# Optimization experiments

Hardware: AMD Instinct MI355X
Metric: run time of the kernel (lower is better)

## Reference

```python
import jax, jax.numpy as jnp
import numpy as np

DIM = 1024
HIDDEN = 4096
NUM_EXPERTS = 8
TOP_K = 2


def setup_inputs() -> dict:
    key = jax.random.key(0)
    ks = jax.random.split(key, 7)
    x = jax.random.normal(ks[0], (4, 2048, DIM), dtype=jnp.float32)
    # router Linear(dim, num_experts)
    Wr = jax.random.normal(ks[1], (DIM, NUM_EXPERTS), dtype=jnp.float32) / np.sqrt(DIM)
    br = jnp.zeros((NUM_EXPERTS,), dtype=jnp.float32)
    # stacked expert weights: Linear(dim, hidden) -> GELU -> Linear(hidden, dim)
    W1 = jax.random.normal(ks[2], (NUM_EXPERTS, DIM, HIDDEN), dtype=jnp.float32) / np.sqrt(DIM)
    b1 = jnp.zeros((NUM_EXPERTS, HIDDEN), dtype=jnp.float32)
    W2 = jax.random.normal(ks[3], (NUM_EXPERTS, HIDDEN, DIM), dtype=jnp.float32) / np.sqrt(HIDDEN)
    b2 = jnp.zeros((NUM_EXPERTS, DIM), dtype=jnp.float32)
    return {"x": x, "Wr": Wr, "br": br, "W1": W1, "b1": b1, "W2": W2, "b2": b2}


def reference(x, Wr, br, W1, b1, W2, b2):
    # router: g_x = W_e x ; p = softmax(g_x)
    logits = jnp.einsum('bsd,de->bse', x, Wr) + br            # [B,S,E]
    probs = jax.nn.softmax(logits, axis=-1)
    topk_probs, topk_idx = jax.lax.top_k(probs, TOP_K)        # [B,S,K]
    # dense compute-all-experts (faithful to torch.stack over experts)
    h = jnp.einsum('bsd,edh->bseh', x, W1) + b1               # [B,S,E,H]
    h = jax.nn.gelu(h, approximate=False)                      # torch nn.GELU default = exact erf
    expert_out = jnp.einsum('bseh,ehd->bsed', h, W2) + b2     # [B,S,E,D]
    # gather top-k expert outputs and mix
    selected = jnp.take_along_axis(expert_out, topk_idx[..., None], axis=2)  # [B,S,K,D]
    mixed = jnp.sum(topk_probs[..., None] * selected, axis=2)                # [B,S,D]
    return mixed, logits, probs, topk_idx, topk_probs
```

## Files before the change

### kernel.cpp

```cpp
#include <hip/hip_runtime.h>
#include <hip/hip_bf16.h>
#include <math.h>
#include <stdint.h>

#define DIMD 1024
#define HIDDEN 4096
#define NE 8
#define TOPK_ 2
#define T_TOKENS 8192
#define NROWS (T_TOKENS * TOPK_)
#define BM 128
#define BN 256
#define BK 64
#define MAXTILES (NROWS / BM + NE)
#define TGS 8
#define SPLITK 2

typedef __bf16 bf16_t;
typedef __bf16 bf16x8 __attribute__((ext_vector_type(8)));
typedef float f32x4 __attribute__((ext_vector_type(4)));

__device__ __forceinline__ void glds16(const void* g, void* l) {
    __builtin_amdgcn_global_load_lds(
        (const __attribute__((address_space(1))) unsigned int*)g,
        (__attribute__((address_space(3))) unsigned int*)l, 16, 0, 0);
}

__device__ __forceinline__ bf16x8 ldfrag(const char* lds_, int row, int kelem) {
    int byte = row * 128 + ((kelem * 2) ^ ((row & 7) << 4));
    return *reinterpret_cast<const bf16x8*>(lds_ + byte);
}

__device__ __forceinline__ int xcd_contig(int bid, int nwg) {
    int xcd = bid & 7;
    int lid = bid >> 3;
    int q = nwg >> 3, r = nwg & 7;
    int base = (xcd < r) ? xcd * (q + 1) : r * (q + 1) + (xcd - r) * q;
    return base + lid;
}

#define STAGE6(kb) do { \
    glds16(pa0 + (kb), lds + wid * 1024); \
    glds16(pa1 + (kb), lds + 8192 + wid * 1024); \
    glds16(pb0 + (kb), lds + 16384 + wid * 1024); \
    glds16(pb1 + (kb), lds + 16384 + 8192 + wid * 1024); \
    glds16(pb2 + (kb), lds + 16384 + 16384 + wid * 1024); \
    glds16(pb3 + (kb), lds + 16384 + 24576 + wid * 1024); \
} while (0)

#define COMPUTE() do { \
    _Pragma("unroll") for (int ks_ = 0; ks_ < 2; ++ks_) { \
        int kk_ = ks_ * 32 + k4; \
        bf16x8 b_[4], a_[4]; \
        _Pragma("unroll") for (int n_ = 0; n_ < 4; ++n_) \
            b_[n_] = ldfrag(lds + 16384, wc + n_ * 16 + rr, kk_); \
        _Pragma("unroll") for (int m_ = 0; m_ < 4; ++m_) \
            a_[m_] = ldfrag(lds, wr + m_ * 16 + rr, kk_); \
        _Pragma("unroll") for (int m_ = 0; m_ < 4; ++m_) \
        _Pragma("unroll") for (int n_ = 0; n_ < 4; ++n_) \
            acc[m_][n_] = __builtin_amdgcn_mfma_f32_16x16x32_bf16(a_[m_], b_[n_], acc[m_][n_], 0, 0, 0); \
    } \
} while (0)

#define GEMM_LOOP(nsteps) do { \
    for (int t_ = 0; t_ < (nsteps); ++t_) { \
        STAGE6(t_ * 128); \
        __syncthreads(); \
        COMPUTE(); \
        __syncthreads(); \
    } \
} while (0)

__global__ __launch_bounds__(256) void router_kernel(
    const float* __restrict__ x, const float* __restrict__ Wr, const float* __restrict__ br,
    float* __restrict__ logits, float* __restrict__ probs,
    float* __restrict__ tidx, float* __restrict__ tprob,
    int* __restrict__ cnt, bf16_t* __restrict__ Xb)
{
    int wave = threadIdx.x >> 6;
    int lane = threadIdx.x & 63;
    int t = blockIdx.x * 4 + wave;
    if (t >= T_TOKENS) return;
    const float* xr = x + (size_t)t * DIMD;
    double acc[NE];
#pragma unroll
    for (int e = 0; e < NE; ++e) acc[e] = 0.0;
    for (int i = 0; i < DIMD / 64; ++i) {
        int d = i * 64 + lane;
        double xv = (double)xr[d];
        float4 w0 = *reinterpret_cast<const float4*>(Wr + d * NE);
        float4 w1 = *reinterpret_cast<const float4*>(Wr + d * NE + 4);
        acc[0] += xv * (double)w0.x; acc[1] += xv * (double)w0.y;
        acc[2] += xv * (double)w0.z; acc[3] += xv * (double)w0.w;
        acc[4] += xv * (double)w1.x; acc[5] += xv * (double)w1.y;
        acc[6] += xv * (double)w1.z; acc[7] += xv * (double)w1.w;
    }
#pragma unroll
    for (int s = 32; s >= 1; s >>= 1) {
#pragma unroll
        for (int e = 0; e < NE; ++e) acc[e] += __shfl_xor(acc[e], s, 64);
    }
    if (lane == 0) {
        double lg[NE], mx = -1e300;
#pragma unroll
        for (int e = 0; e < NE; ++e) { lg[e] = acc[e] + (double)br[e]; mx = fmax(mx, lg[e]); }
        int i0 = 0; double l0 = -1e300;
#pragma unroll
        for (int e = 0; e < NE; ++e) { if (lg[e] > l0) { l0 = lg[e]; i0 = e; } }
        int i1 = -1; double l1 = -1e300;
#pragma unroll
        for (int e = 0; e < NE; ++e) { if (e == i0) continue; if (lg[e] > l1) { l1 = lg[e]; i1 = e; } }
        float pe[NE], s = 0.f;
#pragma unroll
        for (int e = 0; e < NE; ++e) { pe[e] = __expf((float)(lg[e] - mx)); s += pe[e]; }
        float inv = 1.f / s;
#pragma unroll
        for (int e = 0; e < NE; ++e) {
            pe[e] *= inv;
            logits[t * NE + e] = (float)lg[e];
            probs[t * NE + e] = pe[e];
        }
        tidx[t * 2 + 0] = (float)i0; tidx[t * 2 + 1] = (float)i1;
        tprob[t * 2 + 0] = pe[i0];   tprob[t * 2 + 1] = pe[i1];
        atomicAdd(&cnt[i0], 1); atomicAdd(&cnt[i1], 1);
    }
#pragma unroll
    for (int j = 0; j < 2; ++j) {
        int i = (j * 64 + lane) * 8;
        float4 a = *reinterpret_cast<const float4*>(xr + i);
        float4 b = *reinterpret_cast<const float4*>(xr + i + 4);
        bf16x8 o;
        o[0] = (bf16_t)a.x; o[1] = (bf16_t)a.y; o[2] = (bf16_t)a.z; o[3] = (bf16_t)a.w;
        o[4] = (bf16_t)b.x; o[5] = (bf16_t)b.y; o[6] = (bf16_t)b.z; o[7] = (bf16_t)b.w;
        *reinterpret_cast<bf16x8*>(Xb + (size_t)t * DIMD + i) = o;
    }
}

__global__ __launch_bounds__(256) void transpose_kernel(
    const float* __restrict__ in, bf16_t* __restrict__ out, int K, int N)
{
    __shared__ float tile[64][33];
    int e = blockIdx.z;
    int k0 = blockIdx.x * 64;
    int n0 = blockIdx.y * 32;
    const float* ip = in + (size_t)e * K * N;
    bf16_t* op = out + (size_t)e * N * K;
    int t = threadIdx.x;
    int r = t >> 2;
    int c = (t & 3) * 8;
    float4 v0 = *reinterpret_cast<const float4*>(ip + (size_t)(k0 + r) * N + n0 + c);
    float4 v1 = *reinterpret_cast<const float4*>(ip + (size_t)(k0 + r) * N + n0 + c + 4);
    tile[r][c] = v0.x; tile[r][c + 1] = v0.y; tile[r][c + 2] = v0.z; tile[r][c + 3] = v0.w;
    tile[r][c + 4] = v1.x; tile[r][c + 5] = v1.y; tile[r][c + 6] = v1.z; tile[r][c + 7] = v1.w;
    __syncthreads();
    int nn = t >> 3;
    int kk = (t & 7) * 8;
    bf16x8 o;
#pragma unroll
    for (int j = 0; j < 8; ++j) o[j] = (bf16_t)tile[kk + j][nn];
    *reinterpret_cast<bf16x8*>(op + (size_t)(n0 + nn) * K + k0 + kk) = o;
}

__global__ __launch_bounds__(256) void prefix_kernel(
    const int* __restrict__ cnt, int* __restrict__ offsets,
    int* __restrict__ tileE, int* __restrict__ tileRow, int* __restrict__ numTiles)
{
    __shared__ int soff[NE + 1], scnt[NE];
    int t = threadIdx.x;
    if (t == 0) {
        int off = 0;
        for (int e = 0; e < NE; ++e) { scnt[e] = cnt[e]; soff[e] = off; off += scnt[e]; }
        soff[NE] = off;
        int nt = 0;
        for (int e = 0; e < NE; ++e) nt += (scnt[e] + BM - 1) / BM;
        *numTiles = nt;
    }
    __syncthreads();
    if (t <= NE) offsets[t] = soff[t];
    if (t < MAXTILES) {
        int acc = 0;
#pragma unroll
        for (int e = 0; e < NE; ++e) {
            int ntE = (scnt[e] + BM - 1) / BM;
            if (t < acc + ntE) { tileE[t] = e; tileRow[t] = soff[e] + (t - acc) * BM; return; }
            acc += ntE;
        }
    }
}

__global__ __launch_bounds__(256) void scatter_kernel(
    const float* __restrict__ tidx, const float* __restrict__ tprob,
    const int* __restrict__ offsets, int* __restrict__ gcursor,
    int* __restrict__ rowToken, float* __restrict__ rowProb)
{
    __shared__ int lcnt[NE], lbase[NE];
    int t = blockIdx.x * 256 + threadIdx.x;
    if (threadIdx.x < NE) lcnt[threadIdx.x] = 0;
    __syncthreads();
    int e0 = (int)tidx[t * 2 + 0], e1 = (int)tidx[t * 2 + 1];
    float p0 = tprob[t * 2 + 0],   p1 = tprob[t * 2 + 1];
    int r0l = atomicAdd(&lcnt[e0], 1);
    int r1l = atomicAdd(&lcnt[e1], 1);
    __syncthreads();
    if (threadIdx.x < NE) lbase[threadIdx.x] = atomicAdd(&gcursor[threadIdx.x], lcnt[threadIdx.x]);
    __syncthreads();
    int r0 = offsets[e0] + lbase[e0] + r0l;
    int r1 = offsets[e1] + lbase[e1] + r1l;
    rowToken[r0] = t; rowProb[r0] = p0;
    rowToken[r1] = t; rowProb[r1] = p1;
}

__global__ __launch_bounds__(512) void ffn1_kernel(
    const bf16_t* __restrict__ Xb, const bf16_t* __restrict__ W1T, const float* __restrict__ b1,
    const int* __restrict__ tileE, const int* __restrict__ tileRow, const int* __restrict__ numTiles,
    const int* __restrict__ offsets, const int* __restrict__ rowToken,
    bf16_t* __restrict__ h, int hc_base, int hc_len, int NB)
{
    int logical = xcd_contig(blockIdx.x, gridDim.x);
    int tg  = logical / (NB * TGS);
    int rem = logical % (NB * TGS);
    int nb  = rem / TGS;
    int ti  = rem % TGS;
    int tile = tg * TGS + ti;
    if (tile >= *numTiles) return;
    int e = tileE[tile];
    int row0 = tileRow[tile];
    int rend = offsets[e + 1];
    int n0 = nb * BN;
    int nglob = hc_base + n0;

    __shared__ __align__(16) char lds[49152];

    int tid = threadIdx.x;
    int lane = tid & 63;
    int wid = tid >> 6;
    int wr = (wid >> 2) * 64;
    int wc = (wid & 3) * 64;
    int rr = lane & 15;
    int k4 = (lane >> 4) * 8;

    int srow = tid >> 3;
    int xc = (((tid & 7) ^ (srow & 7)) << 4);
    const char *pa0, *pa1, *pb0, *pb1, *pb2, *pb3;
    {
        int g0 = row0 + srow;      if (g0 > NROWS - 1) g0 = NROWS - 1;
        int g1 = row0 + 64 + srow; if (g1 > NROWS - 1) g1 = NROWS - 1;
        pa0 = (const char*)(Xb + (size_t)rowToken[g0] * DIMD) + xc;
        pa1 = (const char*)(Xb + (size_t)rowToken[g1] * DIMD) + xc;
        pb0 = (const char*)(W1T + ((size_t)e * HIDDEN + nglob + srow) * DIMD) + xc;
        pb1 = (const char*)(W1T + ((size_t)e * HIDDEN + nglob + 64 + srow) * DIMD) + xc;
        pb2 = (const char*)(W1T + ((size_t)e * HIDDEN + nglob + 128 + srow) * DIMD) + xc;
        pb3 = (const char*)(W1T + ((size_t)e * HIDDEN + nglob + 192 + srow) * DIMD) + xc;
    }

    f32x4 acc[4][4];
#pragma unroll
    for (int i = 0; i < 4; ++i)
#pragma unroll
        for (int j = 0; j < 4; ++j) acc[i][j] = f32x4{0.f, 0.f, 0.f, 0.f};

    GEMM_LOOP(DIMD / BK);

    int crow = (lane >> 4) * 4;
    int ccol = lane & 15;
#pragma unroll
    for (int m = 0; m < 4; ++m) {
#pragma unroll
        for (int n = 0; n < 4; ++n) {
            int col = wc + n * 16 + ccol;
            float bias = b1[e * HIDDEN + nglob + col];
#pragma unroll
            for (int r = 0; r < 4; ++r) {
                int row = row0 + wr + m * 16 + crow + r;
                if (row < rend) {
                    float v = acc[m][n][r] + bias;
                    float g = 0.5f * v * (1.0f + erff(v * 0.70710678118654752f));
                    h[(size_t)row * hc_len + n0 + col] = (bf16_t)g;
                }
            }
        }
    }
}

__global__ __launch_bounds__(512) void ffn2_kernel(
    const bf16_t* __restrict__ h, const bf16_t* __restrict__ W2T, const float* __restrict__ b2,
    const int* __restrict__ tileE, const int* __restrict__ tileRow, const int* __restrict__ numTiles,
    const int* __restrict__ offsets, const int* __restrict__ rowToken, const float* __restrict__ rowProb,
    float* __restrict__ mixed, int hc_base, int hc_len, int add_bias)
{
    const int NB = DIMD / BN;
    int logical = xcd_contig(blockIdx.x, gridDim.x);
    int z = logical / (MAXTILES * NB);
    int rem = logical % (MAXTILES * NB);
    int tile = rem / NB;
    int nb = rem % NB;
    if (tile >= *numTiles) return;
    int e = tileE[tile];
    int row0 = tileRow[tile];
    int rend = offsets[e + 1];
    int n0 = nb * BN;
    int khalf = hc_len / SPLITK;
    int khb = z * khalf * 2;

    __shared__ __align__(16) char lds[49152];

    int tid = threadIdx.x;
    int lane = tid & 63;
    int wid = tid >> 6;
    int wr = (wid >> 2) * 64;
    int wc = (wid & 3) * 64;
    int rr = lane & 15;
    int k4 = (lane >> 4) * 8;

    int srow = tid >> 3;
    int xc = (((tid & 7) ^ (srow & 7)) << 4);
    const char *pa0, *pa1, *pb0, *pb1, *pb2, *pb3;
    {
        int g0 = row0 + srow;      if (g0 > NROWS - 1) g0 = NROWS - 1;
        int g1 = row0 + 64 + srow; if (g1 > NROWS - 1) g1 = NROWS - 1;
        pa0 = (const char*)(h + (size_t)g0 * hc_len) + khb + xc;
        pa1 = (const char*)(h + (size_t)g1 * hc_len) + khb + xc;
        pb0 = (const char*)(W2T + ((size_t)e * DIMD + n0 + srow) * HIDDEN + hc_base) + khb + xc;
        pb1 = (const char*)(W2T + ((size_t)e * DIMD + n0 + 64 + srow) * HIDDEN + hc_base) + khb + xc;
        pb2 = (const char*)(W2T + ((size_t)e * DIMD + n0 + 128 + srow) * HIDDEN + hc_base) + khb + xc;
        pb3 = (const char*)(W2T + ((size_t)e * DIMD + n0 + 192 + srow) * HIDDEN + hc_base) + khb + xc;
    }

    f32x4 acc[4][4];
#pragma unroll
    for (int i = 0; i < 4; ++i)
#pragma unroll
        for (int j = 0; j < 4; ++j) acc[i][j] = f32x4{0.f, 0.f, 0.f, 0.f};

    GEMM_LOOP(khalf / BK);

    int crow = (lane >> 4) * 4;
    int ccol = lane & 15;
    int dobias = add_bias && (z == 0);
#pragma unroll
    for (int m = 0; m < 4; ++m) {
#pragma unroll
        for (int n = 0; n < 4; ++n) {
            int col = wc + n * 16 + ccol;
            int dcol = n0 + col;
            float bias = dobias ? b2[e * DIMD + dcol] : 0.f;
#pragma unroll
            for (int r = 0; r < 4; ++r) {
                int row = row0 + wr + m * 16 + crow + r;
                if (row < rend) {
                    float v = acc[m][n][r] + bias;
                    float p = rowProb[row];
                    int tok = rowToken[row];
                    atomicAdd(&mixed[(size_t)tok * DIMD + dcol], p * v);
                }
            }
        }
    }
}

extern "C" void kernel_launch(void* const* d_in, const int* in_sizes, int n_in,
                              void* d_out, int out_size, void* d_ws, size_t ws_size,
                              hipStream_t stream)
{
    const float* x  = (const float*)d_in[0];
    const float* Wr = (const float*)d_in[1];
    const float* br = (const float*)d_in[2];
    const float* W1 = (const float*)d_in[3];
    const float* b1 = (const float*)d_in[4];
    const float* W2 = (const float*)d_in[5];
    const float* b2 = (const float*)d_in[6];

    float* out = (float*)d_out;
    float* mixed  = out;
    float* logits = out + (size_t)T_TOKENS * DIMD;
    float* probs  = logits + T_TOKENS * NE;
    float* tidx   = probs + T_TOKENS * NE;
    float* tprob  = tidx + T_TOKENS * TOPK_;

    char* p = (char*)d_ws;
    auto alloc = [&](size_t bytes) { char* r = p; p += (bytes + 255) & ~255ull; return r; };
    int*    small    = (int*)alloc(2 * NE * 4);
    int*    cnt      = small;
    int*    gcursor  = small + NE;
    int*    offsets  = (int*)alloc((NE + 1) * 4);
    int*    numTiles = (int*)alloc(4);
    int*    tileE    = (int*)alloc(MAXTILES * 4);
    int*    tileRow  = (int*)alloc(MAXTILES * 4);
    int*    rowToken = (int*)alloc(NROWS * 4);
    float*  rowProb  = (float*)alloc(NROWS * 4);
    bf16_t* W1T      = (bf16_t*)alloc((size_t)NE * HIDDEN * DIMD * 2);
    bf16_t* W2T      = (bf16_t*)alloc((size_t)NE * DIMD * HIDDEN * 2);
    bf16_t* Xb       = (bf16_t*)alloc((size_t)T_TOKENS * DIMD * 2);
    size_t used = (size_t)(p - (char*)d_ws);
    size_t remain = ws_size > used ? ws_size - used : 0;
    int hc = HIDDEN;
    while (hc > 512 && (size_t)NROWS * hc * 2 > remain) hc >>= 1;
    bf16_t* hbuf = (bf16_t*)alloc((size_t)NROWS * hc * 2);

    hipMemsetAsync(small, 0, 2 * NE * 4, stream);
    hipMemsetAsync(mixed, 0, (size_t)T_TOKENS * DIMD * 4, stream);

    router_kernel<<<T_TOKENS / 4, 256, 0, stream>>>(x, Wr, br, logits, probs, tidx, tprob, cnt, Xb);
    transpose_kernel<<<dim3(DIMD / 64, HIDDEN / 32, NE), 256, 0, stream>>>(W1, W1T, DIMD, HIDDEN);
    transpose_kernel<<<dim3(HIDDEN / 64, DIMD / 32, NE), 256, 0, stream>>>(W2, W2T, HIDDEN, DIMD);
    prefix_kernel<<<1, 256, 0, stream>>>(cnt, offsets, tileE, tileRow, numTiles);
    scatter_kernel<<<T_TOKENS / 256, 256, 0, stream>>>(tidx, tprob, offsets, gcursor, rowToken, rowProb);

    for (int c0 = 0; c0 < HIDDEN; c0 += hc) {
        int nb1 = hc / BN;
        ffn1_kernel<<<MAXTILES * nb1, 512, 0, stream>>>(
            Xb, W1T, b1, tileE, tileRow, numTiles, offsets, rowToken, hbuf, c0, hc, nb1);
        ffn2_kernel<<<MAXTILES * (DIMD / BN) * SPLITK, 512, 0, stream>>>(
            hbuf, W2T, b2, tileE, tileRow, numTiles, offsets, rowToken, rowProb,
            mixed, c0, hc, c0 == 0 ? 1 : 0);
    }
}
```

Before: 828.5 us.

## Retile FFN2 to 128x128 with 256 threads, drop hidden chunking, merge transposes

FFN2 now uses a 128x128 output tile computed by 4 waves with 32KB of LDS instead of 256 columns with 8 waves. This doubles the number of workgroups and allows more occupancy per CU. The hidden-dimension chunk loop is removed, so the full hidden buffer is always allocated and each FFN kernel launches once. The two weight transpose launches are merged into one kernel. The risk is that the full h buffer must fit in the workspace, and the smaller tiles lower data reuse per block.

Result: faster. 798.2 us (-3.7%).

```diff
diff --git a/kernel.cpp b/kernel.cpp
--- a/kernel.cpp
+++ b/kernel.cpp
@@ -9,10 +9,12 @@
 #define TOPK_ 2
 #define T_TOKENS 8192
 #define NROWS (T_TOKENS * TOPK_)
-#define BM 128
-#define BN 256
 #define BK 64
-#define MAXTILES (NROWS / BM + NE)
+#define BM1 128
+#define BN1 256
+#define BM2 128
+#define BN2 128
+#define MAXTILES (NROWS / 128 + NE)
 #define TGS 8
 #define SPLITK 2
 
@@ -38,38 +40,6 @@
     int base = (xcd < r) ? xcd * (q + 1) : r * (q + 1) + (xcd - r) * q;
     return base + lid;
 }
-
-#define STAGE6(kb) do { \
-    glds16(pa0 + (kb), lds + wid * 1024); \
-    glds16(pa1 + (kb), lds + 8192 + wid * 1024); \
-    glds16(pb0 + (kb), lds + 16384 + wid * 1024); \
-    glds16(pb1 + (kb), lds + 16384 + 8192 + wid * 1024); \
-    glds16(pb2 + (kb), lds + 16384 + 16384 + wid * 1024); \
-    glds16(pb3 + (kb), lds + 16384 + 24576 + wid * 1024); \
-} while (0)
-
-#define COMPUTE() do { \
-    _Pragma("unroll") for (int ks_ = 0; ks_ < 2; ++ks_) { \
-        int kk_ = ks_ * 32 + k4; \
-        bf16x8 b_[4], a_[4]; \
-        _Pragma("unroll") for (int n_ = 0; n_ < 4; ++n_) \
-            b_[n_] = ldfrag(lds + 16384, wc + n_ * 16 + rr, kk_); \
-        _Pragma("unroll") for (int m_ = 0; m_ < 4; ++m_) \
-            a_[m_] = ldfrag(lds, wr + m_ * 16 + rr, kk_); \
-        _Pragma("unroll") for (int m_ = 0; m_ < 4; ++m_) \
-        _Pragma("unroll") for (int n_ = 0; n_ < 4; ++n_) \
-            acc[m_][n_] = __builtin_amdgcn_mfma_f32_16x16x32_bf16(a_[m_], b_[n_], acc[m_][n_], 0, 0, 0); \
-    } \
-} while (0)
-
-#define GEMM_LOOP(nsteps) do { \
-    for (int t_ = 0; t_ < (nsteps); ++t_) { \
-        STAGE6(t_ * 128); \
-        __syncthreads(); \
-        COMPUTE(); \
-        __syncthreads(); \
-    } \
-} while (0)
 
 __global__ __launch_bounds__(256) void router_kernel(
     const float* __restrict__ x, const float* __restrict__ Wr, const float* __restrict__ br,
@@ -136,13 +106,25 @@
     }
 }
 
-__global__ __launch_bounds__(256) void transpose_kernel(
-    const float* __restrict__ in, bf16_t* __restrict__ out, int K, int N)
-{
+__global__ __launch_bounds__(256) void transpose_all_kernel(
+    const float* __restrict__ W1, const float* __restrict__ W2,
+    bf16_t* __restrict__ W1T, bf16_t* __restrict__ W2T)
+{
+    int bid = blockIdx.x;
+    const float* in; bf16_t* out; int K, N, kt, nt, e;
+    if (bid < 16384) {
+        in = W1; out = W1T; K = DIMD; N = HIDDEN;
+        e = bid >> 11; int rem = bid & 2047;
+        kt = rem & 15; nt = rem >> 4;
+    } else {
+        bid -= 16384;
+        in = W2; out = W2T; K = HIDDEN; N = DIMD;
+        e = bid >> 11; int rem = bid & 2047;
+        kt = rem & 63; nt = rem >> 6;
+    }
     __shared__ float tile[64][33];
-    int e = blockIdx.z;
-    int k0 = blockIdx.x * 64;
-    int n0 = blockIdx.y * 32;
+    int k0 = kt * 64;
+    int n0 = nt * 32;
     const float* ip = in + (size_t)e * K * N;
     bf16_t* op = out + (size_t)e * N * K;
     int t = threadIdx.x;
@@ -172,7 +154,7 @@
         for (int e = 0; e < NE; ++e) { scnt[e] = cnt[e]; soff[e] = off; off += scnt[e]; }
         soff[NE] = off;
         int nt = 0;
-        for (int e = 0; e < NE; ++e) nt += (scnt[e] + BM - 1) / BM;
+        for (int e = 0; e < NE; ++e) nt += (scnt[e] + 127) / 128;
         *numTiles = nt;
     }
     __syncthreads();
@@ -181,8 +163,8 @@
         int acc = 0;
 #pragma unroll
         for (int e = 0; e < NE; ++e) {
-            int ntE = (scnt[e] + BM - 1) / BM;
-            if (t < acc + ntE) { tileE[t] = e; tileRow[t] = soff[e] + (t - acc) * BM; return; }
+            int ntE = (scnt[e] + 127) / 128;
+            if (t < acc + ntE) { tileE[t] = e; tileRow[t] = soff[e] + (t - acc) * 128; return; }
             acc += ntE;
         }
     }
@@ -214,8 +196,9 @@
     const bf16_t* __restrict__ Xb, const bf16_t* __restrict__ W1T, const float* __restrict__ b1,
     const int* __restrict__ tileE, const int* __restrict__ tileRow, const int* __restrict__ numTiles,
     const int* __restrict__ offsets, const int* __restrict__ rowToken,
-    bf16_t* __restrict__ h, int hc_base, int hc_len, int NB)
-{
+    bf16_t* __restrict__ h)
+{
+    const int NB = HIDDEN / BN1;
     int logical = xcd_contig(blockIdx.x, gridDim.x);
     int tg  = logical / (NB * TGS);
     int rem = logical % (NB * TGS);
@@ -226,8 +209,7 @@
     int e = tileE[tile];
     int row0 = tileRow[tile];
     int rend = offsets[e + 1];
-    int n0 = nb * BN;
-    int nglob = hc_base + n0;
+    int n0 = nb * BN1;
 
     __shared__ __align__(16) char lds[49152];
 
@@ -247,10 +229,10 @@
         int g1 = row0 + 64 + srow; if (g1 > NROWS - 1) g1 = NROWS - 1;
         pa0 = (const char*)(Xb + (size_t)rowToken[g0] * DIMD) + xc;
         pa1 = (const char*)(Xb + (size_t)rowToken[g1] * DIMD) + xc;
-        pb0 = (const char*)(W1T + ((size_t)e * HIDDEN + nglob + srow) * DIMD) + xc;
-        pb1 = (const char*)(W1T + ((size_t)e * HIDDEN + nglob + 64 + srow) * DIMD) + xc;
-        pb2 = (const char*)(W1T + ((size_t)e * HIDDEN + nglob + 128 + srow) * DIMD) + xc;
-        pb3 = (const char*)(W1T + ((size_t)e * HIDDEN + nglob + 192 + srow) * DIMD) + xc;
+        pb0 = (const char*)(W1T + ((size_t)e * HIDDEN + n0 + srow) * DIMD) + xc;
+        pb1 = (const char*)(W1T + ((size_t)e * HIDDEN + n0 + 64 + srow) * DIMD) + xc;
+        pb2 = (const char*)(W1T + ((size_t)e * HIDDEN + n0 + 128 + srow) * DIMD) + xc;
+        pb3 = (const char*)(W1T + ((size_t)e * HIDDEN + n0 + 192 + srow) * DIMD) + xc;
     }
 
     f32x4 acc[4][4];
@@ -259,7 +241,31 @@
 #pragma unroll
         for (int j = 0; j < 4; ++j) acc[i][j] = f32x4{0.f, 0.f, 0.f, 0.f};
 
-    GEMM_LOOP(DIMD / BK);
+    for (int t_ = 0; t_ < DIMD / BK; ++t_) {
+        int kb = t_ * 128;
+        glds16(pa0 + kb, lds + wid * 1024);
+        glds16(pa1 + kb, lds + 8192 + wid * 1024);
+        glds16(pb0 + kb, lds + 16384 + wid * 1024);
+        glds16(pb1 + kb, lds + 24576 + wid * 1024);
+        glds16(pb2 + kb, lds + 32768 + wid * 1024);
+        glds16(pb3 + kb, lds + 40960 + wid * 1024);
+        __syncthreads();
+#pragma unroll
+        for (int ks = 0; ks < 2; ++ks) {
+            int kk = ks * 32 + k4;
+            bf16x8 b_[4], a_[4];
+#pragma unroll
+            for (int n = 0; n < 4; ++n) b_[n] = ldfrag(lds + 16384, wc + n * 16 + rr, kk);
+#pragma unroll
+            for (int m = 0; m < 4; ++m) a_[m] = ldfrag(lds, wr + m * 16 + rr, kk);
+#pragma unroll
+            for (int m = 0; m < 4; ++m)
+#pragma unroll
+                for (int n = 0; n < 4; ++n)
+                    acc[m][n] = __builtin_amdgcn_mfma_f32_16x16x32_bf16(a_[m], b_[n], acc[m][n], 0, 0, 0);
+        }
+        __syncthreads();
+    }
 
     int crow = (lane >> 4) * 4;
     int ccol = lane & 15;
@@ -268,27 +274,27 @@
 #pragma unroll
         for (int n = 0; n < 4; ++n) {
             int col = wc + n * 16 + ccol;
-            float bias = b1[e * HIDDEN + nglob + col];
+            float bias = b1[e * HIDDEN + n0 + col];
 #pragma unroll
             for (int r = 0; r < 4; ++r) {
                 int row = row0 + wr + m * 16 + crow + r;
                 if (row < rend) {
                     float v = acc[m][n][r] + bias;
                     float g = 0.5f * v * (1.0f + erff(v * 0.70710678118654752f));
-                    h[(size_t)row * hc_len + n0 + col] = (bf16_t)g;
+                    h[(size_t)row * HIDDEN + n0 + col] = (bf16_t)g;
                 }
             }
         }
     }
 }
 
-__global__ __launch_bounds__(512) void ffn2_kernel(
+__global__ __launch_bounds__(256) void ffn2_kernel(
     const bf16_t* __restrict__ h, const bf16_t* __restrict__ W2T, const float* __restrict__ b2,
     const int* __restrict__ tileE, const int* __restrict__ tileRow, const int* __restrict__ numTiles,
     const int* __restrict__ offsets, const int* __restrict__ rowToken, const float* __restrict__ rowProb,
-    float* __restrict__ mixed, int hc_base, int hc_len, int add_bias)
-{
-    const int NB = DIMD / BN;
+    float* __restrict__ mixed)
+{
+    const int NB = DIMD / BN2;
     int logical = xcd_contig(blockIdx.x, gridDim.x);
     int z = logical / (MAXTILES * NB);
     int rem = logical % (MAXTILES * NB);
@@ -298,32 +304,36 @@
     int e = tileE[tile];
     int row0 = tileRow[tile];
     int rend = offsets[e + 1];
-    int n0 = nb * BN;
-    int khalf = hc_len / SPLITK;
+    int n0 = nb * BN2;
+    const int khalf = HIDDEN / SPLITK;
     int khb = z * khalf * 2;
 
-    __shared__ __align__(16) char lds[49152];
+    __shared__ __align__(16) char lds[32768];
 
     int tid = threadIdx.x;
     int lane = tid & 63;
     int wid = tid >> 6;
-    int wr = (wid >> 2) * 64;
-    int wc = (wid & 3) * 64;
+    int wr = (wid >> 1) * 64;
+    int wc = (wid & 1) * 64;
     int rr = lane & 15;
     int k4 = (lane >> 4) * 8;
 
     int srow = tid >> 3;
     int xc = (((tid & 7) ^ (srow & 7)) << 4);
-    const char *pa0, *pa1, *pb0, *pb1, *pb2, *pb3;
+    const char *pa0, *pa1, *pa2, *pa3, *pb0, *pb1, *pb2, *pb3;
     {
         int g0 = row0 + srow;      if (g0 > NROWS - 1) g0 = NROWS - 1;
-        int g1 = row0 + 64 + srow; if (g1 > NROWS - 1) g1 = NROWS - 1;
-        pa0 = (const char*)(h + (size_t)g0 * hc_len) + khb + xc;
-        pa1 = (const char*)(h + (size_t)g1 * hc_len) + khb + xc;
-        pb0 = (const char*)(W2T + ((size_t)e * DIMD + n0 + srow) * HIDDEN + hc_base) + khb + xc;
-        pb1 = (const char*)(W2T + ((size_t)e * DIMD + n0 + 64 + srow) * HIDDEN + hc_base) + khb + xc;
-        pb2 = (const char*)(W2T + ((size_t)e * DIMD + n0 + 128 + srow) * HIDDEN + hc_base) + khb + xc;
-        pb3 = (const char*)(W2T + ((size_t)e * DIMD + n0 + 192 + srow) * HIDDEN + hc_base) + khb + xc;
+        int g1 = row0 + 32 + srow; if (g1 > NROWS - 1) g1 = NROWS - 1;
+        int g2 = row0 + 64 + srow; if (g2 > NROWS - 1) g2 = NROWS - 1;
+        int g3 = row0 + 96 + srow; if (g3 > NROWS - 1) g3 = NROWS - 1;
+        pa0 = (const char*)(h + (size_t)g0 * HIDDEN) + khb + xc;
+        pa1 = (const char*)(h + (size_t)g1 * HIDDEN) + khb + xc;
+        pa2 = (const char*)(h + (size_t)g2 * HIDDEN) + khb + xc;
+        pa3 = (const char*)(h + (size_t)g3 * HIDDEN) + khb + xc;
+        pb0 = (const char*)(W2T + ((size_t)e * DIMD + n0 + srow) * HIDDEN) + khb + xc;
+        pb1 = (const char*)(W2T + ((size_t)e * DIMD + n0 + 32 + srow) * HIDDEN) + khb + xc;
+        pb2 = (const char*)(W2T + ((size_t)e * DIMD + n0 + 64 + srow) * HIDDEN) + khb + xc;
+        pb3 = (const char*)(W2T + ((size_t)e * DIMD + n0 + 96 + srow) * HIDDEN) + khb + xc;
     }
 
     f32x4 acc[4][4];
@@ -332,11 +342,35 @@
 #pragma unroll
         for (int j = 0; j < 4; ++j) acc[i][j] = f32x4{0.f, 0.f, 0.f, 0.f};
 
-    GEMM_LOOP(khalf / BK);
+    for (int t_ = 0; t_ < khalf / BK; ++t_) {
+        int kb = t_ * 128;
+        char* dA = lds + wid * 1024;
+        char* dB = lds + 16384 + wid * 1024;
+        glds16(pa0 + kb, dA);          glds16(pb0 + kb, dB);
+        glds16(pa1 + kb, dA + 4096);   glds16(pb1 + kb, dB + 4096);
+        glds16(pa2 + kb, dA + 8192);   glds16(pb2 + kb, dB + 8192);
+        glds16(pa3 + kb, dA + 12288);  glds16(pb3 + kb, dB + 12288);
+        __syncthreads();
+#pragma unroll
+        for (int ks = 0; ks < 2; ++ks) {
+            int kk = ks * 32 + k4;
+            bf16x8 a_[4], b_[4];
+#pragma unroll
+            for (int m = 0; m < 4; ++m) a_[m] = ldfrag(lds, wr + m * 16 + rr, kk);
+#pragma unroll
+            for (int n = 0; n < 4; ++n) b_[n] = ldfrag(lds + 16384, wc + n * 16 + rr, kk);
+#pragma unroll
+            for (int m = 0; m < 4; ++m)
+#pragma unroll
+                for (int n = 0; n < 4; ++n)
+                    acc[m][n] = __builtin_amdgcn_mfma_f32_16x16x32_bf16(a_[m], b_[n], acc[m][n], 0, 0, 0);
+        }
+        __syncthreads();
+    }
 
     int crow = (lane >> 4) * 4;
     int ccol = lane & 15;
-    int dobias = add_bias && (z == 0);
+    int dobias = (z == 0);
 #pragma unroll
     for (int m = 0; m < 4; ++m) {
 #pragma unroll
@@ -391,27 +425,18 @@
     bf16_t* W1T      = (bf16_t*)alloc((size_t)NE * HIDDEN * DIMD * 2);
     bf16_t* W2T      = (bf16_t*)alloc((size_t)NE * DIMD * HIDDEN * 2);
     bf16_t* Xb       = (bf16_t*)alloc((size_t)T_TOKENS * DIMD * 2);
-    size_t used = (size_t)(p - (char*)d_ws);
-    size_t remain = ws_size > used ? ws_size - used : 0;
-    int hc = HIDDEN;
-    while (hc > 512 && (size_t)NROWS * hc * 2 > remain) hc >>= 1;
-    bf16_t* hbuf = (bf16_t*)alloc((size_t)NROWS * hc * 2);
+    bf16_t* hbuf     = (bf16_t*)alloc((size_t)NROWS * HIDDEN * 2);
 
     hipMemsetAsync(small, 0, 2 * NE * 4, stream);
     hipMemsetAsync(mixed, 0, (size_t)T_TOKENS * DIMD * 4, stream);
 
     router_kernel<<<T_TOKENS / 4, 256, 0, stream>>>(x, Wr, br, logits, probs, tidx, tprob, cnt, Xb);
-    transpose_kernel<<<dim3(DIMD / 64, HIDDEN / 32, NE), 256, 0, stream>>>(W1, W1T, DIMD, HIDDEN);
-    transpose_kernel<<<dim3(HIDDEN / 64, DIMD / 32, NE), 256, 0, stream>>>(W2, W2T, HIDDEN, DIMD);
+    transpose_all_kernel<<<32768, 256, 0, stream>>>(W1, W2, W1T, W2T);
     prefix_kernel<<<1, 256, 0, stream>>>(cnt, offsets, tileE, tileRow, numTiles);
     scatter_kernel<<<T_TOKENS / 256, 256, 0, stream>>>(tidx, tprob, offsets, gcursor, rowToken, rowProb);
 
-    for (int c0 = 0; c0 < HIDDEN; c0 += hc) {
-        int nb1 = hc / BN;
-        ffn1_kernel<<<MAXTILES * nb1, 512, 0, stream>>>(
-            Xb, W1T, b1, tileE, tileRow, numTiles, offsets, rowToken, hbuf, c0, hc, nb1);
-        ffn2_kernel<<<MAXTILES * (DIMD / BN) * SPLITK, 512, 0, stream>>>(
-            hbuf, W2T, b2, tileE, tileRow, numTiles, offsets, rowToken, rowProb,
-            mixed, c0, hc, c0 == 0 ? 1 : 0);
-    }
-}
+    ffn1_kernel<<<MAXTILES * (HIDDEN / BN1), 512, 0, stream>>>(
+        Xb, W1T, b1, tileE, tileRow, numTiles, offsets, rowToken, hbuf);
+    ffn2_kernel<<<MAXTILES * (DIMD / BN2) * SPLITK, 256, 0, stream>>>(
+        hbuf, W2T, b2, tileE, tileRow, numTiles, offsets, rowToken, rowProb, mixed);
+}
```
